# Kernel tuning notes

Hardware: AMD Instinct MI355X
Metric: run time of the kernel (lower is better)

Reference implementation:

```python
import jax, jax.numpy as jnp
import numpy as np

N = 50000      # nodes
E = 800000     # edges
D = 256        # embed_dim
H = 8          # num_heads
HD = D // H    # head_dim = 32
F = 4 * D      # feedforward_dim = 1024
SCALE = D ** -0.5  # note: module scales by embed_dim**-0.5, not head_dim
EPS = 1e-5


def setup_inputs() -> dict:
    key = jax.random.key(0)
    ks = jax.random.split(key, 10)
    x = jax.random.normal(ks[0], (N, D), dtype=jnp.float32)
    edge_indices = jax.random.randint(ks[1], (2, E), 0, N, dtype=jnp.int32)
    s = 0.02
    return {
        "x": x,
        "edge_indices": edge_indices,
        "w_qkv": jax.random.normal(ks[2], (D, 3 * D), dtype=jnp.float32) * s,
        "b_qkv": jnp.zeros((3 * D,), dtype=jnp.float32),
        "ln1_g": jnp.ones((D,), dtype=jnp.float32),
        "ln1_b": jnp.zeros((D,), dtype=jnp.float32),
        "ln2_g": jnp.ones((D,), dtype=jnp.float32),
        "ln2_b": jnp.zeros((D,), dtype=jnp.float32),
        "w1": jax.random.normal(ks[3], (D, F), dtype=jnp.float32) * s,
        "b1": jnp.zeros((F,), dtype=jnp.float32),
        "w2": jax.random.normal(ks[4], (F, D), dtype=jnp.float32) * s,
        "b2": jnp.zeros((D,), dtype=jnp.float32),
    }


def _layer_norm(x, g, b):
    m = jnp.mean(x, axis=-1, keepdims=True)
    v = jnp.mean((x - m) ** 2, axis=-1, keepdims=True)
    return (x - m) * jax.lax.rsqrt(v + EPS) * g + b


def _self_attention(x, edge_indices, w_qkv, b_qkv):
    qkv = (x @ w_qkv + b_qkv).reshape(N, H, 3 * HD)
    q, k, v = qkv[..., :HD], qkv[..., HD:2 * HD], qkv[..., 2 * HD:]
    rows, cols = edge_indices[0], edge_indices[1]
    # per-edge, per-head attention logits: [E, H]
    alpha = jnp.einsum('ehd,ehd->eh', q[rows], k[cols]) * SCALE
    # sparse softmax over each row (destination node) segment
    m = jax.ops.segment_max(alpha, rows, num_segments=N)       # [N, H]
    ea = jnp.exp(alpha - m[rows])                              # [E, H]
    denom = jax.ops.segment_sum(ea, rows, num_segments=N)      # [N, H]
    w = ea / denom[rows]                                       # [E, H]
    # per-head SpMM: out[r] += w_e * v[c]  -> [N, H, HD]
    out = jax.ops.segment_sum(w[:, :, None] * v[cols], rows, num_segments=N)
    return out.reshape(N, D)


def reference(x, edge_indices, w_qkv, b_qkv, ln1_g, ln1_b, ln2_g, ln2_b, w1, b1, w2, b2):
    # post-norm (norm_first=False), dropout=0
    x = _layer_norm(x + _self_attention(x, edge_indices, w_qkv, b_qkv), ln1_g, ln1_b)
    ffn = jax.nn.relu(x @ w1 + b1) @ w2 + b2
    x = _layer_norm(x + ffn, ln2_g, ln2_b)
    return x
```

## Files before the change

### kernel.cpp

```cpp
#include <hip/hip_runtime.h>
#include <hip/hip_bf16.h>

#define N_NODES 50000
#define E_EDGES 800000
#define D_MODEL 256
#define H_HEADS 8
#define HDIM    32
#define F_FFN   1024
#define ATT_SCALE 0.0625f
#define LN_EPS  1e-5f
#define NB_SCAN 196

typedef __attribute__((ext_vector_type(8))) short bf16x8;
typedef __attribute__((ext_vector_type(8))) unsigned short u16x8;
typedef __attribute__((ext_vector_type(4))) float f32x4;

__device__ __forceinline__ float bf2f(__hip_bfloat16 v) { return __bfloat162float(v); }
__device__ __forceinline__ __hip_bfloat16 f2bf(float v) { return __float2bfloat16(v); }
__device__ __forceinline__ unsigned short bfbits(float f) {
    __hip_bfloat16 h = __float2bfloat16(f);
    return *reinterpret_cast<unsigned short*>(&h);
}

__device__ __forceinline__ void unpack_bf8(uint4 u, float* f) {
    f[0] = __uint_as_float(u.x << 16); f[1] = __uint_as_float(u.x & 0xFFFF0000u);
    f[2] = __uint_as_float(u.y << 16); f[3] = __uint_as_float(u.y & 0xFFFF0000u);
    f[4] = __uint_as_float(u.z << 16); f[5] = __uint_as_float(u.z & 0xFFFF0000u);
    f[6] = __uint_as_float(u.w << 16); f[7] = __uint_as_float(u.w & 0xFFFF0000u);
}

template<int CTRL>
__device__ __forceinline__ float dpp_add(float v) {
    int t = __builtin_amdgcn_update_dpp(0, __float_as_int(v), CTRL, 0xF, 0xF, true);
    return v + __int_as_float(t);
}

__device__ __forceinline__ void load_lds16(const void* g, void* l) {
    __builtin_amdgcn_global_load_lds(
        (const __attribute__((address_space(1))) unsigned*)g,
        (__attribute__((address_space(3))) unsigned*)l, 16, 0, 0);
}


#define PREP_X   3200000
#define PREP_WQ  (768 * 256)
#define PREP_W1  (1024 * 256)
#define PREP_W2  (256 * 1024)
#define PREP_BQ  768
#define PREP_B1  1024
#define PREP_TOT (PREP_X + PREP_WQ + PREP_W1 + PREP_W2 + PREP_BQ + PREP_B1 + N_NODES)
__global__ void prep_kernel(const float* __restrict__ x, unsigned short* __restrict__ xb,
                            const float* __restrict__ wq, __hip_bfloat16* __restrict__ wtq,
                            const float* __restrict__ w1, __hip_bfloat16* __restrict__ wt1,
                            const float* __restrict__ w2, __hip_bfloat16* __restrict__ wt2,
                            const float* __restrict__ bq, float* __restrict__ bqp,
                            const float* __restrict__ b1, float* __restrict__ b1p,
                            unsigned* __restrict__ counts, unsigned* __restrict__ cursor) {
    int i = blockIdx.x * blockDim.x + threadIdx.x;
    if (i < PREP_X) {
        float4 v = reinterpret_cast<const float4*>(x)[i];
        ushort4 o;
        o.x = bfbits(v.x); o.y = bfbits(v.y); o.z = bfbits(v.z); o.w = bfbits(v.w);
        reinterpret_cast<ushort4*>(xb)[i] = o;
        return;
    }
    i -= PREP_X;
    if (i < PREP_WQ) {
        int n = i >> 8, k = i & 255;
        int s = n >> 8, prel = n & 255;
        int d = (prel & 192) + ((prel & 15) << 2) + ((prel >> 4) & 3);
        int co = (d >> 5) * 96 + s * 32 + (d & 31);
        wtq[i] = f2bf(wq[(size_t)k * 768 + co]);
        return;
    }
    i -= PREP_WQ;
    if (i < PREP_W1) {
        int n = i >> 8, k = i & 255;
        int f = (n & ~63) + ((n & 15) << 2) + ((n >> 4) & 3);
        wt1[i] = f2bf(w1[(size_t)k * 1024 + f]);
        return;
    }
    i -= PREP_W1;
    if (i < PREP_W2) {
        int n = i >> 10, k = i & 1023;
        wt2[i] = f2bf(w2[(size_t)k * 256 + n]);
        return;
    }
    i -= PREP_W2;
    if (i < PREP_BQ) {
        int s = i >> 8, prel = i & 255;
        int d = (prel & 192) + ((prel & 15) << 2) + ((prel >> 4) & 3);
        bqp[i] = bq[(d >> 5) * 96 + s * 32 + (d & 31)];
        return;
    }
    i -= PREP_BQ;
    if (i < PREP_B1) {
        int f = (i & ~63) + ((i & 15) << 2) + ((i >> 4) & 3);
        b1p[i] = b1[f];
        return;
    }
    i -= PREP_B1;
    if (i < N_NODES) { counts[i] = 0u; cursor[i] = 0u; }
}

template<bool RELU, int EPI>
__global__ __launch_bounds__(256)
void mfma_gemm(const __hip_bfloat16* __restrict__ A,
               const __hip_bfloat16* __restrict__ Wt,
               const float* __restrict__ bias,
               __hip_bfloat16* __restrict__ outp,
               __hip_bfloat16* __restrict__ qb,
               unsigned char* __restrict__ kv8,
               int M, int Ncols, int K) {
    __shared__ short Al[2][128 * 32];
    __shared__ short Bl[2][128 * 32];
    const int t = threadIdx.x;
    const int wave = t >> 6, lane = t & 63;

    unsigned flat = blockIdx.y * gridDim.x + blockIdx.x;
    unsigned nwg = gridDim.x * gridDim.y;
    unsigned q8 = nwg >> 3, r8 = nwg & 7;
    unsigned xcd = flat & 7, pos = flat >> 3;
    unsigned wg = (xcd < r8) ? (xcd * (q8 + 1) + pos)
                             : (r8 * (q8 + 1) + (xcd - r8) * q8 + pos);
    const int m0 = (int)(wg / gridDim.x) * 128;
    const int n0 = (int)(wg % gridDim.x) * 128;

    const int wr = wave >> 1, wc = wave & 1;

    const int srow = lane >> 2;
    const int skp  = (lane & 3) ^ ((lane >> 3) & 3);
    const int c0 = wave * 2;
    int ar0 = m0 + c0 * 16 + srow;      if (ar0 >= M) ar0 = M - 1;
    int ar1 = m0 + c0 * 16 + 16 + srow; if (ar1 >= M) ar1 = M - 1;
    const __hip_bfloat16* ga0 = A + (size_t)ar0 * K + skp * 8;
    const __hip_bfloat16* ga1 = A + (size_t)ar1 * K + skp * 8;
    const __hip_bfloat16* gb0 = Wt + (size_t)(n0 + c0 * 16 + srow) * K + skp * 8;
    const __hip_bfloat16* gb1 = Wt + (size_t)(n0 + c0 * 16 + 16 + srow) * K + skp * 8;

    const int lh = lane & 15, q = lane >> 4;
    const int qs = q ^ ((lane >> 1) & 3);
    const short* fa0 = &Al[0][(wr * 64 + lh) * 32 + qs * 8];
    const short* fb0 = &Bl[0][(wc * 64 + lh) * 32 + qs * 8];
    const short* fa1 = &Al[1][(wr * 64 + lh) * 32 + qs * 8];
    const short* fb1 = &Bl[1][(wc * 64 + lh) * 32 + qs * 8];

    f32x4 acc[4][4] = {};

#define GSTAGE(B)                                    \
    load_lds16(ga0, &Al[B][c0 * 512]);               \
    load_lds16(ga1, &Al[B][c0 * 512 + 512]);         \
    load_lds16(gb0, &Bl[B][c0 * 512]);               \
    load_lds16(gb1, &Bl[B][c0 * 512 + 512]);         \
    ga0 += 32; ga1 += 32; gb0 += 32; gb1 += 32;

#define GSTEP(FA, FB)                                                       \
    {                                                                       \
        bf16x8 af[4], bfr[4];                                               \
        _Pragma("unroll")                                                   \
        for (int i = 0; i < 4; i++) {                                       \
            af[i]  = *reinterpret_cast<const bf16x8*>((FA) + i * 16 * 32);  \
            bfr[i] = *reinterpret_cast<const bf16x8*>((FB) + i * 16 * 32);  \
        }                                                                   \
        _Pragma("unroll")                                                   \
        for (int mi = 0; mi < 4; mi++)                                      \
            _Pragma("unroll")                                               \
            for (int nj = 0; nj < 4; nj++)                                  \
                acc[mi][nj] = __builtin_amdgcn_mfma_f32_16x16x32_bf16(      \
                    af[mi], bfr[nj], acc[mi][nj], 0, 0, 0);                 \
    }

    const int nsteps = K >> 5;
    GSTAGE(0)
    __syncthreads();
    for (int s = 0; s < nsteps; s += 2) {
        if (s + 1 < nsteps) { GSTAGE(1) }
        GSTEP(fa0, fb0)
        __syncthreads();
        if (s + 2 < nsteps) { GSTAGE(0) }
        GSTEP(fa1, fb1)
        __syncthreads();
    }
#undef GSTAGE
#undef GSTEP

    const int B = n0 + wc * 64;
    const int gnbase = B + lh;
    float bv[4];
#pragma unroll
    for (int nj = 0; nj < 4; nj++) bv[nj] = bias[gnbase + nj * 16];

    if (EPI == 0) {
        const int sec = B >> 8;
        const int c = ((B & 255) >> 6) * 16 + lh;
#pragma unroll
        for (int mi = 0; mi < 4; mi++) {
            int gmb = m0 + wr * 64 + mi * 16 + q * 4;
#pragma unroll
            for (int r = 0; r < 4; r++) {
                int gm = gmb + r;
                if (gm >= M) continue;
                float v0 = acc[mi][0][r] + bv[0];
                float v1 = acc[mi][1][r] + bv[1];
                float v2 = acc[mi][2][r] + bv[2];
                float v3 = acc[mi][3][r] + bv[3];
                if (sec == 0) {
                    ushort4 o;
                    o.x = bfbits(v0); o.y = bfbits(v1); o.z = bfbits(v2); o.w = bfbits(v3);
                    *reinterpret_cast<ushort4*>(qb + (size_t)gm * 256 + c * 4) = o;
                } else {
                    unsigned u = (unsigned)__builtin_amdgcn_cvt_pk_fp8_f32(v0, v1, 0, false);
                    u = (unsigned)__builtin_amdgcn_cvt_pk_fp8_f32(v2, v3, (int)u, true);
                    *reinterpret_cast<unsigned*>(
                        kv8 + (size_t)gm * 512 + c * 8 + (sec == 1 ? 0 : 4)) = u;
                }
            }
        }
    } else {
        const int cb = B + lh * 4;
#pragma unroll
        for (int mi = 0; mi < 4; mi++) {
            int gmb = m0 + wr * 64 + mi * 16 + q * 4;
#pragma unroll
            for (int r = 0; r < 4; r++) {
                int gm = gmb + r;
                if (gm >= M) continue;
                float v0 = acc[mi][0][r] + bv[0];
                float v1 = acc[mi][1][r] + bv[1];
                float v2 = acc[mi][2][r] + bv[2];
                float v3 = acc[mi][3][r] + bv[3];
                if (RELU) {
                    v0 = fmaxf(v0, 0.f); v1 = fmaxf(v1, 0.f);
                    v2 = fmaxf(v2, 0.f); v3 = fmaxf(v3, 0.f);
                }
                ushort4 o;
                o.x = bfbits(v0); o.y = bfbits(v1); o.z = bfbits(v2); o.w = bfbits(v3);
                *reinterpret_cast<ushort4*>(outp + (size_t)gm * Ncols + cb) = o;
            }
        }
    }
}

__global__ __launch_bounds__(512)
void ffn2_ln_kernel(const __hip_bfloat16* __restrict__ A,
                    const __hip_bfloat16* __restrict__ Wt,
                    const float* __restrict__ bias,
                    const __hip_bfloat16* __restrict__ resid,
                    const float* __restrict__ g, const float* __restrict__ bb,
                    float* __restrict__ out, int M) {
    __shared__ short LDS[2][(64 + 256) * 32];
    const int t = threadIdx.x;
    const int wave = t >> 6, lane = t & 63;
    const int m0 = blockIdx.x * 64;
    const int wr = wave >> 2, wc = wave & 3;

    const int srow = lane >> 2;
    const int skp  = (lane & 3) ^ ((lane >> 3) & 3);

    const __hip_bfloat16* gsrc0; int loff0;
    const __hip_bfloat16* gsrc1; int loff1;
    const __hip_bfloat16* gsrc2; int loff2;
    {
#define STAGE_INIT(GS, LO, C)                                            \
        if ((C) < 4) {                                                   \
            int r_ = m0 + (C) * 16 + srow; if (r_ >= M) r_ = M - 1;      \
            GS = A + (size_t)r_ * 1024 + skp * 8;                        \
            LO = (C) * 512;                                              \
        } else {                                                         \
            GS = Wt + (size_t)(((C) - 4) * 16 + srow) * 1024 + skp * 8;  \
            LO = 2048 + ((C) - 4) * 512;                                 \
        }
        STAGE_INIT(gsrc0, loff0, wave)
        STAGE_INIT(gsrc1, loff1, wave + 8)
        int c2 = (wave < 4) ? wave + 16 : 16;
        STAGE_INIT(gsrc2, loff2, c2)
#undef STAGE_INIT
    }

    const int lh = lane & 15, q = lane >> 4;
    const int qs = q ^ ((lane >> 1) & 3);
    const short* fa0 = &LDS[0][(wr * 32 + lh) * 32 + qs * 8];
    const short* fb0 = &LDS[0][2048 + (wc * 64 + lh) * 32 + qs * 8];
    const short* fa1 = &LDS[1][(wr * 32 + lh) * 32 + qs * 8];
    const short* fb1 = &LDS[1][2048 + (wc * 64 + lh) * 32 + qs * 8];

    f32x4 acc[2][4] = {};

#define FFN2_STAGE(BUF)                                      \
    load_lds16(gsrc0, &LDS[BUF][loff0]);                     \
    load_lds16(gsrc1, &LDS[BUF][loff1]);                     \
    if (wave < 4) load_lds16(gsrc2, &LDS[BUF][loff2]);       \
    gsrc0 += 32; gsrc1 += 32; gsrc2 += 32;

#define FFN2_STEP(FA, FB)                                                   \
    {                                                                       \
        bf16x8 af[2], bfr[4];                                               \
        _Pragma("unroll")                                                   \
        for (int i = 0; i < 2; i++)                                         \
            af[i] = *reinterpret_cast<const bf16x8*>((FA) + i * 16 * 32);   \
        _Pragma("unroll")                                                   \
        for (int i = 0; i < 4; i++)                                         \
            bfr[i] = *reinterpret_cast<const bf16x8*>((FB) + i * 16 * 32);  \
        _Pragma("unroll")                                                   \
        for (int mi = 0; mi < 2; mi++)                                      \
            _Pragma("unroll")                                               \
            for (int nj = 0; nj < 4; nj++)                                  \
                acc[mi][nj] = __builtin_amdgcn_mfma_f32_16x16x32_bf16(      \
                    af[mi], bfr[nj], acc[mi][nj], 0, 0, 0);                 \
    }

    FFN2_STAGE(0)
    __syncthreads();

    for (int s = 0; s < 32; s += 2) {
        FFN2_STAGE(1)
        FFN2_STEP(fa0, fb0)
        __syncthreads();
        if (s < 30) { FFN2_STAGE(0) }
        FFN2_STEP(fa1, fb1)
        __syncthreads();
    }
#undef FFN2_STAGE
#undef FFN2_STEP

    const int colbase = wc * 64 + lh;
    float bv[4], gv[4], bbv[4];
#pragma unroll
    for (int nj = 0; nj < 4; nj++) {
        bv[nj]  = bias[colbase + nj * 16];
        gv[nj]  = g[colbase + nj * 16];
        bbv[nj] = bb[colbase + nj * 16];
    }

    float ps[2][4], pq[2][4];
#pragma unroll
    for (int mi = 0; mi < 2; mi++) {
#pragma unroll
        for (int r = 0; r < 4; r++) {
            int gm = m0 + wr * 32 + mi * 16 + q * 4 + r;
            int rgm = (gm < M) ? gm : M - 1;
            float s = 0.f, s2 = 0.f;
#pragma unroll
            for (int nj = 0; nj < 4; nj++) {
                float v = acc[mi][nj][r] + bv[nj]
                        + bf2f(resid[(size_t)rgm * 256 + colbase + nj * 16]);
                acc[mi][nj][r] = v;
                s += v; s2 += v * v;
            }
            ps[mi][r] = s; pq[mi][r] = s2;
        }
    }
#pragma unroll
    for (int off = 1; off <= 8; off <<= 1) {
#pragma unroll
        for (int mi = 0; mi < 2; mi++)
#pragma unroll
            for (int r = 0; r < 4; r++) {
                ps[mi][r] += __shfl_xor(ps[mi][r], off);
                pq[mi][r] += __shfl_xor(pq[mi][r], off);
            }
    }
    float* rs = (float*)(&LDS[0][0]);
    float* rq = rs + 256;
    if (lh == 0) {
#pragma unroll
        for (int mi = 0; mi < 2; mi++)
#pragma unroll
            for (int r = 0; r < 4; r++) {
                int m = wr * 32 + mi * 16 + q * 4 + r;
                rs[m * 4 + wc] = ps[mi][r];
                rq[m * 4 + wc] = pq[mi][r];
            }
    }
    __syncthreads();

#pragma unroll
    for (int mi = 0; mi < 2; mi++) {
#pragma unroll
        for (int r = 0; r < 4; r++) {
            int m = wr * 32 + mi * 16 + q * 4 + r;
            int gm = m0 + m;
            if (gm >= M) continue;
            float4 rsv = *reinterpret_cast<const float4*>(&rs[m * 4]);
            float4 rqv = *reinterpret_cast<const float4*>(&rq[m * 4]);
            float S  = (rsv.x + rsv.y) + (rsv.z + rsv.w);
            float S2 = (rqv.x + rqv.y) + (rqv.z + rqv.w);
            float mean = S * (1.f / (float)D_MODEL);
            float var  = S2 * (1.f / (float)D_MODEL) - mean * mean;
            float inv  = rsqrtf(var + LN_EPS);
#pragma unroll
            for (int nj = 0; nj < 4; nj++)
                out[(size_t)gm * 256 + colbase + nj * 16] =
                    (acc[mi][nj][r] - mean) * inv * gv[nj] + bbv[nj];
        }
    }
}

__global__ void count_kernel(const int* __restrict__ rows, unsigned* __restrict__ counts) {
    int e = blockIdx.x * blockDim.x + threadIdx.x;
    if (e < E_EDGES) atomicAdd(&counts[rows[e]], 1u);
}

__global__ void scan_blk_kernel(const unsigned* __restrict__ counts,
                                unsigned* __restrict__ offs, unsigned* __restrict__ bsum) {
    __shared__ unsigned sh[256];
    int t = threadIdx.x;
    int i = blockIdx.x * 256 + t;
    unsigned v = (i < N_NODES) ? counts[i] : 0u;
    sh[t] = v;
    __syncthreads();
#pragma unroll
    for (int off = 1; off < 256; off <<= 1) {
        unsigned u = (t >= off) ? sh[t - off] : 0u;
        __syncthreads();
        sh[t] += u;
        __syncthreads();
    }
    if (i < N_NODES) offs[i] = sh[t] - v;
    if (t == 255) bsum[blockIdx.x] = sh[255];
}

__global__ void scan_top_kernel(const unsigned* __restrict__ bsum, unsigned* __restrict__ bpre) {
    __shared__ unsigned sh[256];
    int t = threadIdx.x;
    unsigned v = (t < NB_SCAN) ? bsum[t] : 0u;
    sh[t] = v;
    __syncthreads();
#pragma unroll
    for (int off = 1; off < 256; off <<= 1) {
        unsigned u = (t >= off) ? sh[t - off] : 0u;
        __syncthreads();
        sh[t] += u;
        __syncthreads();
    }
    if (t < NB_SCAN) bpre[t] = sh[t] - v;
    if (t == NB_SCAN - 1) bpre[NB_SCAN] = sh[t];
}

__global__ void scan_add_kernel(unsigned* __restrict__ offs, const unsigned* __restrict__ bpre) {
    int i = blockIdx.x * 256 + threadIdx.x;
    if (i < N_NODES) offs[i] += bpre[blockIdx.x];
    if (i == 0) offs[N_NODES] = bpre[NB_SCAN];
}

__global__ void scatter_kernel(const int* __restrict__ rows, const int* __restrict__ cols,
                               const unsigned* __restrict__ offsets, unsigned* __restrict__ cursor,
                               int* __restrict__ scol) {
    int e = blockIdx.x * blockDim.x + threadIdx.x;
    if (e >= E_EDGES) return;
    int r = rows[e];
    unsigned idx = atomicAdd(&cursor[r], 1u);
    scol[offsets[r] + idx] = cols[e];
}

__global__ __launch_bounds__(128)
void att_agg_kernel(const __hip_bfloat16* __restrict__ qb,
                    const unsigned char* __restrict__ kv8,
                    const unsigned* __restrict__ offsets,
                    const int* __restrict__ scol,
                    const __hip_bfloat16* __restrict__ xres,
                    const float* __restrict__ g, const float* __restrict__ bb,
                    __hip_bfloat16* __restrict__ xn) {
    int n = blockIdx.x * 2 + (threadIdx.x >> 6);
    if (n >= N_NODES) return;
    const int lam = threadIdx.x & 63;
    const int hl  = lam & 31;
    const int sel = lam >> 5;
    const unsigned hlb = hl * 16;
    unsigned beg = offsets[n], end = offsets[n + 1];

    float qv[8];
    {
        uint4 u = *reinterpret_cast<const uint4*>(qb + (size_t)n * 256 + hl * 8);
        unpack_bf8(u, qv);
#pragma unroll
        for (int i = 0; i < 8; i++) qv[i] *= ATT_SCALE;
    }

    float acc[8] = {};
    float l = 0.f;

#define PAIR_BODY(W, VMUL)                                                      \
    {                                                                           \
        auto k01 = __builtin_amdgcn_cvt_pk_f32_fp8((int)(W).x, false);          \
        auto k23 = __builtin_amdgcn_cvt_pk_f32_fp8((int)(W).x, true);           \
        auto k45 = __builtin_amdgcn_cvt_pk_f32_fp8((int)(W).z, false);          \
        auto k67 = __builtin_amdgcn_cvt_pk_f32_fp8((int)(W).z, true);           \
        float sv = qv[0] * k01[0] + qv[1] * k01[1] + qv[2] * k23[0]             \
                 + qv[3] * k23[1] + qv[4] * k45[0] + qv[5] * k45[1]             \
                 + qv[6] * k67[0] + qv[7] * k67[1];                             \
        sv = dpp_add<0xB1>(sv);                           \
        sv = dpp_add<0x4E>(sv);                           \
        float pv = __expf(sv) * (VMUL);                                         \
        l += pv;                                                                \
        auto v01 = __builtin_amdgcn_cvt_pk_f32_fp8((int)(W).y, false);          \
        auto v23 = __builtin_amdgcn_cvt_pk_f32_fp8((int)(W).y, true);           \
        auto v45 = __builtin_amdgcn_cvt_pk_f32_fp8((int)(W).w, false);          \
        auto v67 = __builtin_amdgcn_cvt_pk_f32_fp8((int)(W).w, true);           \
        acc[0] += pv * v01[0]; acc[1] += pv * v01[1];                           \
        acc[2] += pv * v23[0]; acc[3] += pv * v23[1];                           \
        acc[4] += pv * v45[0]; acc[5] += pv * v45[1];                           \
        acc[6] += pv * v67[0]; acc[7] += pv * v67[1];                           \
    }

    unsigned e = beg;
    unsigned oA = 0, oB = 0, oC = 0, oD = 0;
    if (e + 8 <= end) {
        oA = ((unsigned)scol[e + sel])     << 9;
        oB = ((unsigned)scol[e + 2 + sel]) << 9;
        oC = ((unsigned)scol[e + 4 + sel]) << 9;
        oD = ((unsigned)scol[e + 6 + sel]) << 9;
    }
    while (e + 8 <= end) {
        uint4 wa = *reinterpret_cast<const uint4*>(kv8 + (oA + hlb));
        uint4 wb = *reinterpret_cast<const uint4*>(kv8 + (oB + hlb));
        uint4 wc = *reinterpret_cast<const uint4*>(kv8 + (oC + hlb));
        uint4 wd = *reinterpret_cast<const uint4*>(kv8 + (oD + hlb));
        e += 8;
        if (e + 8 <= end) {
            oA = ((unsigned)scol[e + sel])     << 9;
            oB = ((unsigned)scol[e + 2 + sel]) << 9;
            oC = ((unsigned)scol[e + 4 + sel]) << 9;
            oD = ((unsigned)scol[e + 6 + sel]) << 9;
        }
        PAIR_BODY(wa, 1.0f)
        PAIR_BODY(wb, 1.0f)
        PAIR_BODY(wc, 1.0f)
        PAIR_BODY(wd, 1.0f)
    }
    for (; e + 2 <= end; e += 2) {
        unsigned o0 = ((unsigned)scol[e + sel]) << 9;
        uint4 wa = *reinterpret_cast<const uint4*>(kv8 + (o0 + hlb));
        PAIR_BODY(wa, 1.0f)
    }
    if (e < end) {
        unsigned o0 = ((unsigned)scol[e]) << 9;
        uint4 wa = *reinterpret_cast<const uint4*>(kv8 + (o0 + hlb));
        PAIR_BODY(wa, sel ? 0.0f : 1.0f)
    }
#undef PAIR_BODY

    l += __shfl_xor(l, 32);
#pragma unroll
    for (int i = 0; i < 8; i++) acc[i] += __shfl_xor(acc[i], 32);

    float inv_l = (l > 0.f) ? 1.f / l : 0.f;

    float tv[8];
    {
        float xv[8];
        uint4 u = *reinterpret_cast<const uint4*>(xres + (size_t)n * D_MODEL + hl * 8);
        unpack_bf8(u, xv);
#pragma unroll
        for (int i = 0; i < 8; i++) tv[i] = acc[i] * inv_l + xv[i];
    }

    float s = 0.f, s2 = 0.f;
#pragma unroll
    for (int i = 0; i < 8; i++) { s += tv[i]; s2 += tv[i] * tv[i]; }
#pragma unroll
    for (int off = 1; off <= 16; off <<= 1) {
        s  += __shfl_xor(s, off);
        s2 += __shfl_xor(s2, off);
    }
    float mean = s * (1.f / (float)D_MODEL);
    float var  = s2 * (1.f / (float)D_MODEL) - mean * mean;
    float inv  = rsqrtf(var + LN_EPS);

    if (sel == 0) {
        const float4* gp = reinterpret_cast<const float4*>(g);
        const float4* bp = reinterpret_cast<const float4*>(bb);
        float4 g0 = gp[hl * 2], g1 = gp[hl * 2 + 1];
        float4 b0 = bp[hl * 2], b1 = bp[hl * 2 + 1];
        float gv[8] = {g0.x, g0.y, g0.z, g0.w, g1.x, g1.y, g1.z, g1.w};
        float bv[8] = {b0.x, b0.y, b0.z, b0.w, b1.x, b1.y, b1.z, b1.w};
        u16x8 o;
#pragma unroll
        for (int i = 0; i < 8; i++)
            o[i] = bfbits((tv[i] - mean) * inv * gv[i] + bv[i]);
        *reinterpret_cast<u16x8*>(xn + (size_t)n * D_MODEL + hl * 8) = o;
    }
}

extern "C" void kernel_launch(void* const* d_in, const int* in_sizes, int n_in,
                              void* d_out, int out_size, void* d_ws, size_t ws_size,
                              hipStream_t stream) {
    const float* x     = (const float*)d_in[0];
    const int*   ei    = (const int*)d_in[1];
    const float* w_qkv = (const float*)d_in[2];
    const float* b_qkv = (const float*)d_in[3];
    const float* ln1_g = (const float*)d_in[4];
    const float* ln1_b = (const float*)d_in[5];
    const float* ln2_g = (const float*)d_in[6];
    const float* ln2_b = (const float*)d_in[7];
    const float* w1    = (const float*)d_in[8];
    const float* b1    = (const float*)d_in[9];
    const float* w2    = (const float*)d_in[10];
    const float* b2    = (const float*)d_in[11];
    const int* rows = ei;
    const int* cols = ei + E_EDGES;

    char* ws = (char*)d_ws;
    __hip_bfloat16* qb      = (__hip_bfloat16*)(ws + 0);
    unsigned char*  kv8     = (unsigned char*)(ws + 25600000);
    __hip_bfloat16* hbuf    = (__hip_bfloat16*)(ws + 0);
    __hip_bfloat16* xb      = (__hip_bfloat16*)(ws + 102400000);
    __hip_bfloat16* wtq     = (__hip_bfloat16*)(ws + 128000000);
    __hip_bfloat16* wt1     = (__hip_bfloat16*)(ws + 128400000);
    __hip_bfloat16* wt2     = (__hip_bfloat16*)(ws + 129000000);
    unsigned*       counts  = (unsigned*)(ws + 129600000);
    unsigned*       offsets = (unsigned*)(ws + 129800000);
    unsigned*       cursor  = (unsigned*)(ws + 130000008);
    int*            scol    = (int*)(ws + 130200008);
    unsigned*       bsum    = (unsigned*)(ws + 133400008);
    unsigned*       bpre    = (unsigned*)(ws + 133401032);
    float*          bqp     = (float*)(ws + 133500000);
    float*          b1p     = (float*)(ws + 133510000);
    __hip_bfloat16* xn      = (__hip_bfloat16*)(ws + 153600000);

    const int nbM = (N_NODES + 127) / 128;

    prep_kernel<<<(PREP_TOT + 255) / 256, 256, 0, stream>>>(
        x, (unsigned short*)xb, w_qkv, wtq, w1, wt1, w2, wt2,
        b_qkv, bqp, b1, b1p, counts, cursor);

    mfma_gemm<false, 0><<<dim3(768 / 128, nbM), 256, 0, stream>>>(
        xb, wtq, bqp, nullptr, qb, kv8, N_NODES, 768, D_MODEL);

    count_kernel<<<(E_EDGES + 255) / 256, 256, 0, stream>>>(rows, counts);
    scan_blk_kernel<<<NB_SCAN, 256, 0, stream>>>(counts, offsets, bsum);
    scan_top_kernel<<<1, 256, 0, stream>>>(bsum, bpre);
    scan_add_kernel<<<NB_SCAN, 256, 0, stream>>>(offsets, bpre);
    scatter_kernel<<<(E_EDGES + 255) / 256, 256, 0, stream>>>(rows, cols, offsets, cursor, scol);

    att_agg_kernel<<<(N_NODES + 1) / 2, 128, 0, stream>>>(qb, kv8, offsets, scol,
                                                          xb, ln1_g, ln1_b, xn);

    mfma_gemm<true, 1><<<dim3(F_FFN / 128, nbM), 256, 0, stream>>>(
        xn, wt1, b1p, hbuf, nullptr, nullptr, N_NODES, F_FFN, D_MODEL);

    ffn2_ln_kernel<<<(N_NODES + 63) / 64, 512, 0, stream>>>(hbuf, wt2, b2, xn, ln2_g, ln2_b,
                                                            (float*)d_out, N_NODES);
}
```

Measured before the change: 410.7 us.

## Triple-buffer GEMM K-loops with vmcnt waits and drop the scan_add kernel

Both MFMA GEMMs (QKV/FFN1 and the FFN2+LN kernel) move from double to triple-buffered LDS staging. Each step now uses one barrier plus explicit vmcnt waits, so global-to-LDS loads run two stages ahead, and K becomes a template constant so the loop fully unrolls. The separate scan_add kernel is removed: consumers add the block prefix bpre to the local offsets when they read them, which saves one launch. In exchange, LDS use per block rises, which may lower occupancy, and the hand-counted vmcnt values must match the number of loads each wave issues per stage.

```diff
diff --git a/kernel.cpp b/kernel.cpp
--- a/kernel.cpp
+++ b/kernel.cpp
@@ -40,6 +40,10 @@
         (const __attribute__((address_space(1))) unsigned*)g,
         (__attribute__((address_space(3))) unsigned*)l, 16, 0, 0);
 }
+
+#define WAITV(N) asm volatile("s_waitcnt vmcnt(" #N ")" ::: "memory")
+#define SBAR()   { __builtin_amdgcn_sched_barrier(0); __builtin_amdgcn_s_barrier(); \
+                   __builtin_amdgcn_sched_barrier(0); }
 
 
 #define PREP_X   3200000
@@ -103,7 +107,7 @@
     if (i < N_NODES) { counts[i] = 0u; cursor[i] = 0u; }
 }
 
-template<bool RELU, int EPI>
+template<bool RELU, int EPI, int KT>
 __global__ __launch_bounds__(256)
 void mfma_gemm(const __hip_bfloat16* __restrict__ A,
                const __hip_bfloat16* __restrict__ Wt,
@@ -111,9 +115,9 @@
                __hip_bfloat16* __restrict__ outp,
                __hip_bfloat16* __restrict__ qb,
                unsigned char* __restrict__ kv8,
-               int M, int Ncols, int K) {
-    __shared__ short Al[2][128 * 32];
-    __shared__ short Bl[2][128 * 32];
+               int M, int Ncols) {
+    __shared__ short Al[3][128 * 32];
+    __shared__ short Bl[3][128 * 32];
     const int t = threadIdx.x;
     const int wave = t >> 6, lane = t & 63;
 
@@ -133,17 +137,15 @@
     const int c0 = wave * 2;
     int ar0 = m0 + c0 * 16 + srow;      if (ar0 >= M) ar0 = M - 1;
     int ar1 = m0 + c0 * 16 + 16 + srow; if (ar1 >= M) ar1 = M - 1;
-    const __hip_bfloat16* ga0 = A + (size_t)ar0 * K + skp * 8;
-    const __hip_bfloat16* ga1 = A + (size_t)ar1 * K + skp * 8;
-    const __hip_bfloat16* gb0 = Wt + (size_t)(n0 + c0 * 16 + srow) * K + skp * 8;
-    const __hip_bfloat16* gb1 = Wt + (size_t)(n0 + c0 * 16 + 16 + srow) * K + skp * 8;
+    const __hip_bfloat16* ga0 = A + (size_t)ar0 * KT + skp * 8;
+    const __hip_bfloat16* ga1 = A + (size_t)ar1 * KT + skp * 8;
+    const __hip_bfloat16* gb0 = Wt + (size_t)(n0 + c0 * 16 + srow) * KT + skp * 8;
+    const __hip_bfloat16* gb1 = Wt + (size_t)(n0 + c0 * 16 + 16 + srow) * KT + skp * 8;
 
     const int lh = lane & 15, q = lane >> 4;
     const int qs = q ^ ((lane >> 1) & 3);
-    const short* fa0 = &Al[0][(wr * 64 + lh) * 32 + qs * 8];
-    const short* fb0 = &Bl[0][(wc * 64 + lh) * 32 + qs * 8];
-    const short* fa1 = &Al[1][(wr * 64 + lh) * 32 + qs * 8];
-    const short* fb1 = &Bl[1][(wc * 64 + lh) * 32 + qs * 8];
+    const short* faB = &Al[0][(wr * 64 + lh) * 32 + qs * 8];
+    const short* fbB = &Bl[0][(wc * 64 + lh) * 32 + qs * 8];
 
     f32x4 acc[4][4] = {};
 
@@ -170,16 +172,23 @@
                     af[mi], bfr[nj], acc[mi][nj], 0, 0, 0);                 \
     }
 
-    const int nsteps = K >> 5;
+    constexpr int ns = KT >> 5;
     GSTAGE(0)
-    __syncthreads();
-    for (int s = 0; s < nsteps; s += 2) {
-        if (s + 1 < nsteps) { GSTAGE(1) }
-        GSTEP(fa0, fb0)
-        __syncthreads();
-        if (s + 2 < nsteps) { GSTAGE(0) }
-        GSTEP(fa1, fb1)
-        __syncthreads();
+    GSTAGE(1)
+#pragma unroll
+    for (int s = 0; s < ns; ++s) {
+        if (s < ns - 1) { WAITV(4); } else { WAITV(0); }
+        SBAR();
+        if (s + 2 < ns) {
+            switch ((s + 2) % 3) {
+                case 0: { GSTAGE(0) } break;
+                case 1: { GSTAGE(1) } break;
+                default: { GSTAGE(2) } break;
+            }
+        }
+        const short* fa = faB + (s % 3) * 4096;
+        const short* fb = fbB + (s % 3) * 4096;
+        GSTEP(fa, fb)
     }
 #undef GSTAGE
 #undef GSTEP
@@ -248,7 +257,7 @@
                     const __hip_bfloat16* __restrict__ resid,
                     const float* __restrict__ g, const float* __restrict__ bb,
                     float* __restrict__ out, int M) {
-    __shared__ short LDS[2][(64 + 256) * 32];
+    __shared__ short LDS[3][(64 + 256) * 32];
     const int t = threadIdx.x;
     const int wave = t >> 6, lane = t & 63;
     const int m0 = blockIdx.x * 64;
@@ -279,10 +288,8 @@
 
     const int lh = lane & 15, q = lane >> 4;
     const int qs = q ^ ((lane >> 1) & 3);
-    const short* fa0 = &LDS[0][(wr * 32 + lh) * 32 + qs * 8];
-    const short* fb0 = &LDS[0][2048 + (wc * 64 + lh) * 32 + qs * 8];
-    const short* fa1 = &LDS[1][(wr * 32 + lh) * 32 + qs * 8];
-    const short* fb1 = &LDS[1][2048 + (wc * 64 + lh) * 32 + qs * 8];
+    const short* faB = &LDS[0][(wr * 32 + lh) * 32 + qs * 8];
+    const short* fbB = &LDS[0][2048 + (wc * 64 + lh) * 32 + qs * 8];
 
     f32x4 acc[2][4] = {};
 
@@ -310,16 +317,28 @@
     }
 
     FFN2_STAGE(0)
-    __syncthreads();
-
-    for (int s = 0; s < 32; s += 2) {
-        FFN2_STAGE(1)
-        FFN2_STEP(fa0, fb0)
-        __syncthreads();
-        if (s < 30) { FFN2_STAGE(0) }
-        FFN2_STEP(fa1, fb1)
-        __syncthreads();
-    }
+    FFN2_STAGE(1)
+#pragma unroll
+    for (int s = 0; s < 32; ++s) {
+        if (s < 31) {
+            if (wave < 4) { WAITV(3); } else { WAITV(2); }
+        } else {
+            WAITV(0);
+        }
+        SBAR();
+        if (s + 2 < 32) {
+            switch ((s + 2) % 3) {
+                case 0: { FFN2_STAGE(0) } break;
+                case 1: { FFN2_STAGE(1) } break;
+                default: { FFN2_STAGE(2) } break;
+            }
+        }
+        const short* fa = faB + (s % 3) * 10240;
+        const short* fb = fbB + (s % 3) * 10240;
+        FFN2_STEP(fa, fb)
+    }
+    WAITV(0);
+    SBAR();
 #undef FFN2_STAGE
 #undef FFN2_STEP
 
@@ -437,26 +456,23 @@
     if (t == NB_SCAN - 1) bpre[NB_SCAN] = sh[t];
 }
 
-__global__ void scan_add_kernel(unsigned* __restrict__ offs, const unsigned* __restrict__ bpre) {
-    int i = blockIdx.x * 256 + threadIdx.x;
-    if (i < N_NODES) offs[i] += bpre[blockIdx.x];
-    if (i == 0) offs[N_NODES] = bpre[NB_SCAN];
-}
-
 __global__ void scatter_kernel(const int* __restrict__ rows, const int* __restrict__ cols,
-                               const unsigned* __restrict__ offsets, unsigned* __restrict__ cursor,
+                               const unsigned* __restrict__ offsets,
+                               const unsigned* __restrict__ bpre,
+                               unsigned* __restrict__ cursor,
                                int* __restrict__ scol) {
     int e = blockIdx.x * blockDim.x + threadIdx.x;
     if (e >= E_EDGES) return;
     int r = rows[e];
     unsigned idx = atomicAdd(&cursor[r], 1u);
-    scol[offsets[r] + idx] = cols[e];
+    scol[offsets[r] + bpre[r >> 8] + idx] = cols[e];
 }
 
 __global__ __launch_bounds__(128)
 void att_agg_kernel(const __hip_bfloat16* __restrict__ qb,
                     const unsigned char* __restrict__ kv8,
                     const unsigned* __restrict__ offsets,
+                    const unsigned* __restrict__ bpre,
                     const int* __restrict__ scol,
                     const __hip_bfloat16* __restrict__ xres,
                     const float* __restrict__ g, const float* __restrict__ bb,
@@ -467,7 +483,9 @@
     const int hl  = lam & 31;
     const int sel = lam >> 5;
     const unsigned hlb = hl * 16;
-    unsigned beg = offsets[n], end = offsets[n + 1];
+    unsigned beg = offsets[n] + bpre[n >> 8];
+    unsigned end = (n + 1 == N_NODES) ? bpre[NB_SCAN]
+                                      : offsets[n + 1] + bpre[(n + 1) >> 8];
 
     float qv[8];
     {
@@ -624,20 +642,20 @@
         x, (unsigned short*)xb, w_qkv, wtq, w1, wt1, w2, wt2,
         b_qkv, bqp, b1, b1p, counts, cursor);
 
-    mfma_gemm<false, 0><<<dim3(768 / 128, nbM), 256, 0, stream>>>(
-        xb, wtq, bqp, nullptr, qb, kv8, N_NODES, 768, D_MODEL);
+    mfma_gemm<false, 0, 256><<<dim3(768 / 128, nbM), 256, 0, stream>>>(
+        xb, wtq, bqp, nullptr, qb, kv8, N_NODES, 768);
 
     count_kernel<<<(E_EDGES + 255) / 256, 256, 0, stream>>>(rows, counts);
     scan_blk_kernel<<<NB_SCAN, 256, 0, stream>>>(counts, offsets, bsum);
     scan_top_kernel<<<1, 256, 0, stream>>>(bsum, bpre);
-    scan_add_kernel<<<NB_SCAN, 256, 0, stream>>>(offsets, bpre);
-    scatter_kernel<<<(E_EDGES + 255) / 256, 256, 0, stream>>>(rows, cols, offsets, cursor, scol);
-
-    att_agg_kernel<<<(N_NODES + 1) / 2, 128, 0, stream>>>(qb, kv8, offsets, scol,
+    scatter_kernel<<<(E_EDGES + 255) / 256, 256, 0, stream>>>(rows, cols, offsets, bpre,
+                                                              cursor, scol);
+
+    att_agg_kernel<<<(N_NODES + 1) / 2, 128, 0, stream>>>(qb, kv8, offsets, bpre, scol,
                                                           xb, ln1_g, ln1_b, xn);
 
-    mfma_gemm<true, 1><<<dim3(F_FFN / 128, nbM), 256, 0, stream>>>(
-        xn, wt1, b1p, hbuf, nullptr, nullptr, N_NODES, F_FFN, D_MODEL);
+    mfma_gemm<true, 1, 256><<<dim3(F_FFN / 128, nbM), 256, 0, stream>>>(
+        xn, wt1, b1p, hbuf, nullptr, nullptr, N_NODES, F_FFN);
 
     ffn2_ln_kernel<<<(N_NODES + 63) / 64, 512, 0, stream>>>(hbuf, wt2, b2, xn, ln2_g, ln2_b,
                                                             (float*)d_out, N_NODES);
```

Result: no change. 409.2 us (-0.4%).
